# Performance work log

Hardware: AMD Instinct MI355X
Metric: run time of the kernel (lower is better)

Reference implementation:

```python
import jax, jax.numpy as jnp
import numpy as np
import math

D_MODEL = 768
N_HEAD = 12
D_FF = 3072
LN_EPS = 1e-5


def gelu_new(x):
    return 0.5 * x * (1.0 + jnp.tanh(jnp.sqrt(2.0 / jnp.pi) * (x + 0.044715 * x ** 3)))


def layer_norm(x, g, b):
    mu = jnp.mean(x, axis=-1, keepdims=True)
    var = jnp.mean(jnp.square(x - mu), axis=-1, keepdims=True)
    return (x - mu) * jax.lax.rsqrt(var + LN_EPS) * g + b


def setup_inputs() -> dict:
    key = jax.random.key(0)
    ks = jax.random.split(key, 8)
    B, S = 4, 2048
    x = jax.random.normal(ks[0], (B, S, D_MODEL), dtype=jnp.float32)
    # causal look-ahead mask: 1 = attend, 0 = masked
    look_ahead_mask = jnp.tril(jnp.ones((S, S), dtype=jnp.float32))[None, None]
    std = 0.02
    Wqkv = jax.random.normal(ks[1], (D_MODEL, 3 * D_MODEL), dtype=jnp.float32) * std
    bqkv = jnp.zeros((3 * D_MODEL,), dtype=jnp.float32)
    Wo = jax.random.normal(ks[2], (D_MODEL, D_MODEL), dtype=jnp.float32) * std
    bo = jnp.zeros((D_MODEL,), dtype=jnp.float32)
    Wfc = jax.random.normal(ks[3], (D_MODEL, D_FF), dtype=jnp.float32) * std
    bfc = jnp.zeros((D_FF,), dtype=jnp.float32)
    Wpr = jax.random.normal(ks[4], (D_FF, D_MODEL), dtype=jnp.float32) * std
    bpr = jnp.zeros((D_MODEL,), dtype=jnp.float32)
    g1 = jnp.ones((D_MODEL,), dtype=jnp.float32)
    b1 = jnp.zeros((D_MODEL,), dtype=jnp.float32)
    g2 = jnp.ones((D_MODEL,), dtype=jnp.float32)
    b2 = jnp.zeros((D_MODEL,), dtype=jnp.float32)
    return dict(x=x, look_ahead_mask=look_ahead_mask, Wqkv=Wqkv, bqkv=bqkv,
                Wo=Wo, bo=bo, Wfc=Wfc, bfc=bfc, Wpr=Wpr, bpr=bpr,
                g1=g1, b1=b1, g2=g2, b2=b2)


def reference(x, look_ahead_mask, Wqkv, bqkv, Wo, bo, Wfc, bfc, Wpr, bpr, g1, b1, g2, b2):
    B, S, D = x.shape
    dk = D // N_HEAD
    # --- attention sublayer (dropout = identity, eval mode) ---
    nx = layer_norm(x, g1, b1)
    qkv = nx @ Wqkv + bqkv                       # [B,S,3D]
    q, k, v = jnp.split(qkv, 3, axis=-1)
    def heads(t):
        return t.reshape(B, S, N_HEAD, dk).transpose(0, 2, 1, 3)  # [B,H,S,dk]
    q, k, v = heads(q), heads(k), heads(v)
    scores = jnp.einsum('bhqd,bhkd->bhqk', q, k) / jnp.sqrt(jnp.float32(dk))
    scores = scores + (1.0 - look_ahead_mask) * -10000.0
    attn_scores = jax.nn.softmax(scores, axis=-1)  # [B,H,S,S]
    out = jnp.einsum('bhqk,bhkd->bhqd', attn_scores, v)
    out = out.transpose(0, 2, 1, 3).reshape(B, S, D)
    a = out @ Wo + bo
    x = x + a
    # --- MLP sublayer ---
    h = layer_norm(x, g2, b2)
    m = gelu_new(h @ Wfc + bfc) @ Wpr + bpr
    x = x + m
    return (x, attn_scores)
```

## Files before the change

### kernel.cpp

```cpp
#include <hip/hip_runtime.h>
#include <stdint.h>

#define D_MODEL 768
#define NHEAD   12
#define DKH     64
#define SEQ     2048
#define BATCH   4
#define DFF     3072
#define NROWS   (BATCH*SEQ)

typedef __bf16 bf16x8 __attribute__((ext_vector_type(8)));
typedef float  f32x4  __attribute__((ext_vector_type(4)));

__device__ __forceinline__ unsigned short f2bf(float f) {
  union { float f; unsigned int u; } v; v.f = f;
  unsigned int r = v.u + 0x7fffu + ((v.u >> 16) & 1u);
  return (unsigned short)(r >> 16);
}

__device__ __forceinline__ void gl_lds16(const void* g, void* l) {
  __builtin_amdgcn_global_load_lds(
      (__attribute__((address_space(1))) void*)(uintptr_t)g,
      (__attribute__((address_space(3))) void*)(uintptr_t)l, 16, 0, 0);
}

__global__ __launch_bounds__(256) void k_prep(
    const float* __restrict__ Wqkv, const float* __restrict__ Wo,
    const float* __restrict__ Wfc, const float* __restrict__ Wpr,
    unsigned short* __restrict__ WqkvT, unsigned short* __restrict__ WoT,
    unsigned short* __restrict__ WfcT, unsigned short* __restrict__ WprT,
    const float* __restrict__ x, const float* __restrict__ g1,
    const float* __restrict__ b1, unsigned short* __restrict__ nx) {
  int id = blockIdx.x;
  if (id < NROWS) {
    int row = id, t = threadIdx.x;
    const float* xr = x + (size_t)row * D_MODEL;
    float v0 = xr[t], v1 = xr[t + 256], v2 = xr[t + 512];
    float s = v0 + v1 + v2;
    float s2 = v0 * v0 + v1 * v1 + v2 * v2;
#pragma unroll
    for (int off = 32; off >= 1; off >>= 1) {
      s  += __shfl_xor(s, off, 64);
      s2 += __shfl_xor(s2, off, 64);
    }
    __shared__ float rs_[4], rs2_[4];
    int w = t >> 6;
    if ((t & 63) == 0) { rs_[w] = s; rs2_[w] = s2; }
    __syncthreads();
    s  = rs_[0] + rs_[1] + rs_[2] + rs_[3];
    s2 = rs2_[0] + rs2_[1] + rs2_[2] + rs2_[3];
    float mu  = s * (1.0f / D_MODEL);
    float var = s2 * (1.0f / D_MODEL) - mu * mu;
    float rstd = rsqrtf(var + 1e-5f);
    unsigned short* yr = nx + (size_t)row * D_MODEL;
    yr[t]       = f2bf((v0 - mu) * rstd * g1[t]       + b1[t]);
    yr[t + 256] = f2bf((v1 - mu) * rstd * g1[t + 256] + b1[t + 256]);
    yr[t + 512] = f2bf((v2 - mu) * rstd * g1[t + 512] + b1[t + 512]);
  } else {
    int wid = id - NROWS;
    const float* W; unsigned short* Wt; int K, N, tid;
    if (wid < 1728)      { W = Wqkv; Wt = WqkvT; K = 768;  N = 2304; tid = wid; }
    else if (wid < 2304) { W = Wo;   Wt = WoT;   K = 768;  N = 768;  tid = wid - 1728; }
    else if (wid < 4608) { W = Wfc;  Wt = WfcT;  K = 768;  N = 3072; tid = wid - 2304; }
    else                 { W = Wpr;  Wt = WprT;  K = 3072; N = 768;  tid = wid - 4608; }
    int ntn = N / 32;
    int n0 = (tid % ntn) * 32, k0 = (tid / ntn) * 32;

    __shared__ float tile[32][33];
    int c = threadIdx.x & 31, r = threadIdx.x >> 5;
#pragma unroll
    for (int i = 0; i < 4; ++i)
      tile[r + i * 8][c] = W[(size_t)(k0 + r + i * 8) * N + n0 + c];
    __syncthreads();
#pragma unroll
    for (int i = 0; i < 4; ++i)
      Wt[(size_t)(n0 + r + i * 8) * K + k0 + c] = f2bf(tile[c][r + i * 8]);
  }
}

__global__ __launch_bounds__(256) void k_ln(const float* __restrict__ x,
                                            const float* __restrict__ g,
                                            const float* __restrict__ bb,
                                            unsigned short* __restrict__ y) {
  int row = blockIdx.x, t = threadIdx.x;
  const float* xr = x + (size_t)row * D_MODEL;
  float v0 = xr[t], v1 = xr[t + 256], v2 = xr[t + 512];
  float s = v0 + v1 + v2;
  float s2 = v0 * v0 + v1 * v1 + v2 * v2;
#pragma unroll
  for (int off = 32; off >= 1; off >>= 1) {
    s  += __shfl_xor(s, off, 64);
    s2 += __shfl_xor(s2, off, 64);
  }
  __shared__ float rs_[4], rs2_[4];
  int w = t >> 6;
  if ((t & 63) == 0) { rs_[w] = s; rs2_[w] = s2; }
  __syncthreads();
  s  = rs_[0] + rs_[1] + rs_[2] + rs_[3];
  s2 = rs2_[0] + rs2_[1] + rs2_[2] + rs2_[3];
  float mu  = s * (1.0f / D_MODEL);
  float var = s2 * (1.0f / D_MODEL) - mu * mu;
  float rstd = rsqrtf(var + 1e-5f);
  unsigned short* yr = y + (size_t)row * D_MODEL;
  yr[t]       = f2bf((v0 - mu) * rstd * g[t]       + bb[t]);
  yr[t + 256] = f2bf((v1 - mu) * rstd * g[t + 256] + bb[t + 256]);
  yr[t + 512] = f2bf((v2 - mu) * rstd * g[t + 512] + bb[t + 512]);
}

#define EPI_QKV 0
#define EPI_WO  1
#define EPI_FC  2
#define EPI_PR  3

template <int EPI>
__global__ __launch_bounds__(256) void k_gemm(
    const unsigned short* __restrict__ A,
    const unsigned short* __restrict__ Bt,
    const float* __restrict__ bias,
    const float* __restrict__ res,
    float* __restrict__ outf,
    unsigned short* __restrict__ outb,
    unsigned short* __restrict__ qo,
    unsigned short* __restrict__ ko,
    unsigned short* __restrict__ vto,
    int K, int N) {
  __shared__ __align__(16) unsigned char smem[36864];
  unsigned short* As = (unsigned short*)smem;
  unsigned short* Bs = (unsigned short*)(smem + 16384);
  int t = threadIdx.x;
  int l = t & 63, w = t >> 6;
  int wm = w >> 1, wn = w & 1;

  int gx = gridDim.x;
  int nwg = gx * gridDim.y;
  int orig = blockIdx.y * gx + blockIdx.x;
  int wg = (orig & 7) * (nwg >> 3) + (orig >> 3);
  int bx = wg % gx, by = wg / gx;
  int m0 = by * 128, n0 = bx * 128;
  int lr = l & 15, lg = l >> 4;

  const f32x4 fz = {0.0f, 0.0f, 0.0f, 0.0f};
  f32x4 acc[4][4];
#pragma unroll
  for (int i = 0; i < 4; ++i)
#pragma unroll
    for (int j = 0; j < 4; ++j) acc[i][j] = fz;

  int arow = t >> 3;
  int aslot = t & 7;
  const unsigned short* Ag = A + (size_t)(m0 + arow) * K + aslot * 8;
  const unsigned short* Bg = Bt + (size_t)(n0 + arow) * K + aslot * 8;
  int ntile = K >> 6;

  for (int kt = 0; kt < ntile; ++kt) {
    const unsigned short* Agk = Ag + kt * 64;
    const unsigned short* Bgk = Bg + kt * 64;
#pragma unroll
    for (int i = 0; i < 4; ++i)
      gl_lds16(Agk + (size_t)i * 32 * K, As + (i * 256 + t) * 8);
#pragma unroll
    for (int i = 0; i < 4; ++i)
      gl_lds16(Bgk + (size_t)i * 32 * K, Bs + (i * 256 + t) * 8);
    __syncthreads();
#pragma unroll
    for (int ks = 0; ks < 2; ++ks) {
      bf16x8 af[4], bf_[4];
#pragma unroll
      for (int i = 0; i < 4; ++i)
        af[i] = *(const bf16x8*)(As + (wm * 64 + i * 16 + lr) * 64 + ks * 32 + lg * 8);
#pragma unroll
      for (int i = 0; i < 4; ++i)
        bf_[i] = *(const bf16x8*)(Bs + (wn * 64 + i * 16 + lr) * 64 + ks * 32 + lg * 8);
#pragma unroll
      for (int i = 0; i < 4; ++i)
#pragma unroll
        for (int j = 0; j < 4; ++j)
          acc[i][j] = __builtin_amdgcn_mfma_f32_16x16x32_bf16(af[i], bf_[j], acc[i][j], 0, 0, 0);
    }
    __syncthreads();
  }

  int mb = m0 + wm * 64;
  int nb = n0 + wn * 64;

  if constexpr (EPI == EPI_WO || EPI == EPI_PR) {
#pragma unroll
    for (int i = 0; i < 4; ++i)
#pragma unroll
      for (int r = 0; r < 4; ++r) {
        int m = mb + i * 16 + 4 * lg + r;
#pragma unroll
        for (int j = 0; j < 4; ++j) {
          int n = nb + j * 16 + lr;
          outf[(size_t)m * D_MODEL + n] = acc[i][j][r] + bias[n] + res[(size_t)m * D_MODEL + n];
        }
      }
  } else if constexpr (EPI == EPI_FC) {
#pragma unroll
    for (int i = 0; i < 4; ++i)
#pragma unroll
      for (int r = 0; r < 4; ++r) {
        int m = mb + i * 16 + 4 * lg + r;
#pragma unroll
        for (int j = 0; j < 4; ++j) {
          int n = nb + j * 16 + lr;
          float u = acc[i][j][r] + bias[n];
          float c = 0.7978845608028654f * (u + 0.044715f * u * u * u);
          float a2 = fabsf(c);
          float e = __expf(-2.0f * a2);
          float th = (1.0f - e) / (1.0f + e);
          th = (c < 0.0f) ? -th : th;
          outb[(size_t)m * DFF + n] = f2bf(0.5f * u * (1.0f + th));
        }
      }
  } else {
    int region = n0 / 768;
    int b = m0 >> 11;
    if (region < 2) {
      unsigned short* dst = (region == 0) ? qo : ko;
#pragma unroll
      for (int i = 0; i < 4; ++i)
#pragma unroll
        for (int r = 0; r < 4; ++r) {
          int m = mb + i * 16 + 4 * lg + r;
          int s = m & (SEQ - 1);
#pragma unroll
          for (int j = 0; j < 4; ++j) {
            int n = nb + j * 16 + lr;
            int nl = n - region * 768;
            int h = nl >> 6, d = nl & 63;
            dst[(((size_t)(b * NHEAD + h) * SEQ + s) << 6) + d] = f2bf(acc[i][j][r] + bias[n]);
          }
        }
    } else {
      int nl = nb - 1536;
      int h = nl >> 6;
      unsigned short* Tw = (unsigned short*)(smem + w * 9216);
#pragma unroll
      for (int j = 0; j < 4; ++j) {
        int dcol = j * 16 + lr;
        int n = nb + j * 16 + lr;
#pragma unroll
        for (int i = 0; i < 4; ++i)
#pragma unroll
          for (int r = 0; r < 4; ++r)
            Tw[dcol * 72 + i * 16 + 4 * lg + r] = f2bf(acc[i][j][r] + bias[n]);
      }
      __syncthreads();
      int srow = l >> 3, sc = (l & 7) * 8;
      int s0 = mb & (SEQ - 1);
#pragma unroll
      for (int i = 0; i < 8; ++i) {
        int d = i * 8 + srow;
        bf16x8 vv = *(const bf16x8*)(Tw + d * 72 + sc);
        *(bf16x8*)(vto + ((size_t)(b * NHEAD + h) * DKH + d) * SEQ + s0 + sc) = vv;
      }
    }
  }
}

template <int EPI>
__global__ __launch_bounds__(256) void k_gemm_pw(
    const unsigned short* __restrict__ A,
    const unsigned short* __restrict__ Bt,
    const float* __restrict__ bias,
    const float* __restrict__ res,
    float* __restrict__ outf,
    unsigned short* __restrict__ outb,
    int K, int N,
    int npw, int gxe, int pwoff,
    const unsigned short* __restrict__ qp,
    const unsigned short* __restrict__ kp,
    const float* __restrict__ lsumbuf,
    float* __restrict__ attn) {
  __shared__ __align__(16) unsigned char smem[36864];
  int t = threadIdx.x;
  int l = t & 63, w = t >> 6;
  int lr = l & 15, lg = l >> 4;
  const f32x4 fz = {0.0f, 0.0f, 0.0f, 0.0f};

  if ((int)blockIdx.x < npw) {
    unsigned short* Ks = (unsigned short*)smem;
    int idx = blockIdx.x + pwoff;
    int qt = 31 - (idx & 31);
    int bh = idx >> 5;
    int qrow0 = qt * 64 + w * 16;

    const unsigned short* qbase = qp + ((size_t)bh * SEQ + qrow0 + lr) * DKH;
    bf16x8 aq0 = *(const bf16x8*)(qbase + lg * 8);
    bf16x8 aq1 = *(const bf16x8*)(qbase + 32 + lg * 8);

    float invl[4];
#pragma unroll
    for (int r = 0; r < 4; ++r)
      invl[r] = 1.0f / lsumbuf[(size_t)bh * SEQ + qrow0 + 4 * lg + r];

    for (int kt = 0; kt <= qt; ++kt) {
#pragma unroll
      for (int i = 0; i < 2; ++i) {
        int lin = i * 256 + t;
        gl_lds16(kp + ((size_t)bh * SEQ + kt * 64 + (lin >> 3)) * DKH + (lin & 7) * 8,
                 Ks + lin * 8);
      }
      __syncthreads();
      f32x4 sacc[4];
#pragma unroll
      for (int f = 0; f < 4; ++f) sacc[f] = fz;
#pragma unroll
      for (int f = 0; f < 4; ++f) {
        bf16x8 bk0 = *(const bf16x8*)(Ks + (f * 16 + lr) * 64 + lg * 8);
        sacc[f] = __builtin_amdgcn_mfma_f32_16x16x32_bf16(aq0, bk0, sacc[f], 0, 0, 0);
        bf16x8 bk1 = *(const bf16x8*)(Ks + (f * 16 + lr) * 64 + 32 + lg * 8);
        sacc[f] = __builtin_amdgcn_mfma_f32_16x16x32_bf16(aq1, bk1, sacc[f], 0, 0, 0);
      }
#pragma unroll
      for (int r = 0; r < 4; ++r) {
        int qg = qrow0 + 4 * lg + r;
#pragma unroll
        for (int f = 0; f < 4; ++f) {
          int ksg = kt * 64 + f * 16 + lr;
          float p = (ksg <= qg) ? __expf(sacc[f][r] * 0.125f) * invl[r] : 0.0f;
          __builtin_nontemporal_store(p, &attn[((size_t)bh * SEQ + qg) * SEQ + ksg]);
        }
      }
      __syncthreads();
    }

    int zstart = (qt + 1) * 64;
    const f32x4 z4 = {0.f, 0.f, 0.f, 0.f};
#pragma unroll
    for (int r = 0; r < 4; ++r) {
      int qg = qrow0 + 4 * lg + r;
      float* rowp = attn + ((size_t)bh * SEQ + qg) * SEQ;
      for (int c = zstart + lr * 4; c < SEQ; c += 64)
        __builtin_nontemporal_store(z4, (f32x4*)(rowp + c));
    }
    return;
  }

  unsigned short* As = (unsigned short*)smem;
  unsigned short* Bs = (unsigned short*)(smem + 16384);
  int wm = w >> 1, wn = w & 1;
  int orig = blockIdx.x - npw;
  int ngemm = gridDim.x - npw;
  int wg = (orig & 7) * (ngemm >> 3) + (orig >> 3);
  int bx = wg % gxe, by = wg / gxe;
  int m0 = by * 128, n0 = bx * 128;

  f32x4 acc[4][4];
#pragma unroll
  for (int i = 0; i < 4; ++i)
#pragma unroll
    for (int j = 0; j < 4; ++j) acc[i][j] = fz;

  int arow = t >> 3;
  int aslot = t & 7;
  const unsigned short* Ag = A + (size_t)(m0 + arow) * K + aslot * 8;
  const unsigned short* Bg = Bt + (size_t)(n0 + arow) * K + aslot * 8;
  int ntile = K >> 6;

  for (int kt = 0; kt < ntile; ++kt) {
    const unsigned short* Agk = Ag + kt * 64;
    const unsigned short* Bgk = Bg + kt * 64;
#pragma unroll
    for (int i = 0; i < 4; ++i)
      gl_lds16(Agk + (size_t)i * 32 * K, As + (i * 256 + t) * 8);
#pragma unroll
    for (int i = 0; i < 4; ++i)
      gl_lds16(Bgk + (size_t)i * 32 * K, Bs + (i * 256 + t) * 8);
    __syncthreads();
#pragma unroll
    for (int ks = 0; ks < 2; ++ks) {
      bf16x8 af[4], bf_[4];
#pragma unroll
      for (int i = 0; i < 4; ++i)
        af[i] = *(const bf16x8*)(As + (wm * 64 + i * 16 + lr) * 64 + ks * 32 + lg * 8);
#pragma unroll
      for (int i = 0; i < 4; ++i)
        bf_[i] = *(const bf16x8*)(Bs + (wn * 64 + i * 16 + lr) * 64 + ks * 32 + lg * 8);
#pragma unroll
      for (int i = 0; i < 4; ++i)
#pragma unroll
        for (int j = 0; j < 4; ++j)
          acc[i][j] = __builtin_amdgcn_mfma_f32_16x16x32_bf16(af[i], bf_[j], acc[i][j], 0, 0, 0);
    }
    __syncthreads();
  }

  int mb = m0 + wm * 64;
  int nb = n0 + wn * 64;

  if constexpr (EPI == EPI_PR) {
#pragma unroll
    for (int i = 0; i < 4; ++i)
#pragma unroll
      for (int r = 0; r < 4; ++r) {
        int m = mb + i * 16 + 4 * lg + r;
#pragma unroll
        for (int j = 0; j < 4; ++j) {
          int n = nb + j * 16 + lr;
          outf[(size_t)m * D_MODEL + n] = acc[i][j][r] + bias[n] + res[(size_t)m * D_MODEL + n];
        }
      }
  } else {
#pragma unroll
    for (int i = 0; i < 4; ++i)
#pragma unroll
      for (int r = 0; r < 4; ++r) {
        int m = mb + i * 16 + 4 * lg + r;
#pragma unroll
        for (int j = 0; j < 4; ++j) {
          int n = nb + j * 16 + lr;
          float u = acc[i][j][r] + bias[n];
          float c = 0.7978845608028654f * (u + 0.044715f * u * u * u);
          float a2 = fabsf(c);
          float e = __expf(-2.0f * a2);
          float th = (1.0f - e) / (1.0f + e);
          th = (c < 0.0f) ? -th : th;
          outb[(size_t)m * DFF + n] = f2bf(0.5f * u * (1.0f + th));
        }
      }
  }
}

template <int WRITEP>
__global__ __launch_bounds__(256) void k_attn(const unsigned short* __restrict__ q,
                                              const unsigned short* __restrict__ kk,
                                              const unsigned short* __restrict__ vt,
                                              float* __restrict__ lsumbuf,
                                              float* __restrict__ attn,
                                              unsigned short* __restrict__ ao) {
  __shared__ __align__(16) unsigned short Ks[2][64 * 64];
  __shared__ __align__(16) unsigned short Vts[2][64 * 64];
  __shared__ __align__(16) unsigned short Pw[4][32 * 72];
  int t = threadIdx.x, l = t & 63, w = t >> 6;
  int lr = l & 15, lg = l >> 4;
  int qt = gridDim.x - 1 - blockIdx.x;
  int bh = blockIdx.y;
  int q0 = qt * 128;
  int qrow0 = q0 + w * 32;
  int kmax = 2 * qt + 1;

  auto stageK = [&](int kt, int buf) {
#pragma unroll
    for (int i = 0; i < 2; ++i) {
      int lin = i * 256 + t;
      gl_lds16(kk + ((size_t)bh * SEQ + kt * 64 + (lin >> 3)) * DKH + (lin & 7) * 8,
               Ks[buf] + lin * 8);
    }
  };
  auto stageV = [&](int kt, int buf) {
#pragma unroll
    for (int i = 0; i < 2; ++i) {
      int lin = i * 256 + t;
      gl_lds16(vt + ((size_t)bh * DKH + (lin >> 3)) * SEQ + kt * 64 + (lin & 7) * 8,
               Vts[buf] + lin * 8);
    }
  };

  bf16x8 aq[2][2];
#pragma unroll
  for (int m = 0; m < 2; ++m) {
    const unsigned short* qbase = q + ((size_t)bh * SEQ + qrow0 + m * 16 + lr) * DKH;
    aq[m][0] = *(const bf16x8*)(qbase + lg * 8);
    aq[m][1] = *(const bf16x8*)(qbase + 32 + lg * 8);
  }

  const f32x4 fz = {0.0f, 0.0f, 0.0f, 0.0f};
  float lsum[2][4] = {{0.f, 0.f, 0.f, 0.f}, {0.f, 0.f, 0.f, 0.f}};
  f32x4 oacc[2][4];
#pragma unroll
  for (int m = 0; m < 2; ++m)
#pragma unroll
    for (int f = 0; f < 4; ++f) oacc[m][f] = fz;

  unsigned short* Pme = Pw[w];
  stageK(0, 0);
  stageV(0, 0);
  __syncthreads();
  int cur = 0;
  for (int kt = 0; kt <= kmax; ++kt) {
    if (kt < kmax) { stageK(kt + 1, cur ^ 1); stageV(kt + 1, cur ^ 1); }
    const unsigned short* Kc = Ks[cur];
    const unsigned short* Vc = Vts[cur];
#pragma unroll
    for (int m = 0; m < 2; ++m) {
      f32x4 sacc[4];
#pragma unroll
      for (int f = 0; f < 4; ++f) sacc[f] = fz;
#pragma unroll
      for (int f = 0; f < 4; ++f) {
        bf16x8 bk0 = *(const bf16x8*)(Kc + (f * 16 + lr) * 64 + lg * 8);
        sacc[f] = __builtin_amdgcn_mfma_f32_16x16x32_bf16(aq[m][0], bk0, sacc[f], 0, 0, 0);
        bf16x8 bk1 = *(const bf16x8*)(Kc + (f * 16 + lr) * 64 + 32 + lg * 8);
        sacc[f] = __builtin_amdgcn_mfma_f32_16x16x32_bf16(aq[m][1], bk1, sacc[f], 0, 0, 0);
      }
#pragma unroll
      for (int r = 0; r < 4; ++r) {
        int qg = qrow0 + m * 16 + 4 * lg + r;
        float rsum = 0.f;
#pragma unroll
        for (int f = 0; f < 4; ++f) {
          int ksg = kt * 64 + f * 16 + lr;
          float p = (ksg <= qg) ? __expf(sacc[f][r] * 0.125f) : 0.0f;
          rsum += p;
          Pme[(m * 16 + 4 * lg + r) * 72 + f * 16 + lr] = f2bf(p);
        }
        rsum += __shfl_xor(rsum, 1, 64);
        rsum += __shfl_xor(rsum, 2, 64);
        rsum += __shfl_xor(rsum, 4, 64);
        rsum += __shfl_xor(rsum, 8, 64);
        lsum[m][r] += rsum;
      }
    }
#pragma unroll
    for (int ds = 0; ds < 2; ++ds)
#pragma unroll
      for (int m = 0; m < 2; ++m) {
        bf16x8 ap = *(const bf16x8*)(Pme + (m * 16 + lr) * 72 + ds * 32 + lg * 8);
#pragma unroll
        for (int f = 0; f < 4; ++f) {
          bf16x8 bv = *(const bf16x8*)(Vc + (f * 16 + lr) * 64 + ds * 32 + lg * 8);
          oacc[m][f] = __builtin_amdgcn_mfma_f32_16x16x32_bf16(ap, bv, oacc[m][f], 0, 0, 0);
        }
      }
    __syncthreads();
    cur ^= 1;
  }

  float invl[2][4];
#pragma unroll
  for (int m = 0; m < 2; ++m)
#pragma unroll
    for (int r = 0; r < 4; ++r) {
      invl[m][r] = 1.0f / lsum[m][r];
      if (WRITEP == 0 && lr == 0)
        lsumbuf[(size_t)bh * SEQ + qrow0 + m * 16 + 4 * lg + r] = lsum[m][r];
    }

  int b = bh / NHEAD, h = bh % NHEAD;
#pragma unroll
  for (int m = 0; m < 2; ++m)
#pragma unroll
    for (int r = 0; r < 4; ++r) {
      int qg = qrow0 + m * 16 + 4 * lg + r;
#pragma unroll
      for (int f = 0; f < 4; ++f)
        ao[(size_t)(b * SEQ + qg) * D_MODEL + h * DKH + f * 16 + lr] =
            f2bf(oacc[m][f][r] * invl[m][r]);
    }

  if (WRITEP) {
    stageK(0, 0);
    __syncthreads();
    cur = 0;
    for (int kt = 0; kt <= kmax; ++kt) {
      if (kt < kmax) stageK(kt + 1, cur ^ 1);
      const unsigned short* Kc = Ks[cur];
#pragma unroll
      for (int m = 0; m < 2; ++m) {
        f32x4 sacc[4];
#pragma unroll
        for (int f = 0; f < 4; ++f) sacc[f] = fz;
#pragma unroll
        for (int f = 0; f < 4; ++f) {
          bf16x8 bk0 = *(const bf16x8*)(Kc + (f * 16 + lr) * 64 + lg * 8);
          sacc[f] = __builtin_amdgcn_mfma_f32_16x16x32_bf16(aq[m][0], bk0, sacc[f], 0, 0, 0);
          bf16x8 bk1 = *(const bf16x8*)(Kc + (f * 16 + lr) * 64 + 32 + lg * 8);
          sacc[f] = __builtin_amdgcn_mfma_f32_16x16x32_bf16(aq[m][1], bk1, sacc[f], 0, 0, 0);
        }
#pragma unroll
        for (int r = 0; r < 4; ++r) {
          int qg = qrow0 + m * 16 + 4 * lg + r;
#pragma unroll
          for (int f = 0; f < 4; ++f) {
            int ksg = kt * 64 + f * 16 + lr;
            float p = (ksg <= qg) ? __expf(sacc[f][r] * 0.125f) * invl[m][r] : 0.0f;
            __builtin_nontemporal_store(p, &attn[((size_t)bh * SEQ + qg) * SEQ + ksg]);
          }
        }
      }
      __syncthreads();
      cur ^= 1;
    }

    int zstart = q0 + 128;
    const f32x4 z4 = {0.f, 0.f, 0.f, 0.f};
#pragma unroll
    for (int m = 0; m < 2; ++m)
#pragma unroll
      for (int r = 0; r < 4; ++r) {
        int qg = qrow0 + m * 16 + 4 * lg + r;
        float* rowp = attn + ((size_t)bh * SEQ + qg) * SEQ;
        for (int c = zstart + lr * 4; c < SEQ; c += 64)
          __builtin_nontemporal_store(z4, (f32x4*)(rowp + c));
      }
  }
}

__global__ __launch_bounds__(256) void k_pwrite(const unsigned short* __restrict__ q,
                                                const unsigned short* __restrict__ kk,
                                                const float* __restrict__ lsumbuf,
                                                float* __restrict__ attn) {
  __shared__ __align__(16) unsigned short Ks[64 * 64];
  int t = threadIdx.x, l = t & 63, w = t >> 6;
  int lr = l & 15, lg = l >> 4;
  int qt = blockIdx.x, bh = blockIdx.y;
  int qrow0 = qt * 64 + w * 16;

  const unsigned short* qbase = q + ((size_t)bh * SEQ + qrow0 + lr) * DKH;
  bf16x8 aq0 = *(const bf16x8*)(qbase + lg * 8);
  bf16x8 aq1 = *(const bf16x8*)(qbase + 32 + lg * 8);

  float invl[4];
#pragma unroll
  for (int r = 0; r < 4; ++r)
    invl[r] = 1.0f / lsumbuf[(size_t)bh * SEQ + qrow0 + 4 * lg + r];

  const f32x4 fz = {0.0f, 0.0f, 0.0f, 0.0f};
  for (int kt = 0; kt <= qt; ++kt) {
#pragma unroll
    for (int i = 0; i < 2; ++i) {
      int lin = i * 256 + t;
      gl_lds16(kk + ((size_t)bh * SEQ + kt * 64 + (lin >> 3)) * DKH + (lin & 7) * 8,
               Ks + lin * 8);
    }
    __syncthreads();
    f32x4 sacc[4];
#pragma unroll
    for (int f = 0; f < 4; ++f) sacc[f] = fz;
#pragma unroll
    for (int f = 0; f < 4; ++f) {
      bf16x8 bk0 = *(const bf16x8*)(Ks + (f * 16 + lr) * 64 + lg * 8);
      sacc[f] = __builtin_amdgcn_mfma_f32_16x16x32_bf16(aq0, bk0, sacc[f], 0, 0, 0);
      bf16x8 bk1 = *(const bf16x8*)(Ks + (f * 16 + lr) * 64 + 32 + lg * 8);
      sacc[f] = __builtin_amdgcn_mfma_f32_16x16x32_bf16(aq1, bk1, sacc[f], 0, 0, 0);
    }
#pragma unroll
    for (int r = 0; r < 4; ++r) {
      int qg = qrow0 + 4 * lg + r;
#pragma unroll
      for (int f = 0; f < 4; ++f) {
        int ksg = kt * 64 + f * 16 + lr;
        float p = (ksg <= qg) ? __expf(sacc[f][r] * 0.125f) * invl[r] : 0.0f;
        attn[((size_t)bh * SEQ + qg) * SEQ + ksg] = p;
      }
    }
    __syncthreads();
  }

  int zstart = (qt + 1) * 64;
#pragma unroll
  for (int r = 0; r < 4; ++r) {
    int qg = qrow0 + 4 * lg + r;
    float* rowp = attn + ((size_t)bh * SEQ + qg) * SEQ;
    for (int c = zstart + lr * 4; c < SEQ; c += 64)
      *(f32x4*)(rowp + c) = fz;
  }
}

extern "C" void kernel_launch(void* const* d_in, const int* in_sizes, int n_in,
                              void* d_out, int out_size, void* d_ws, size_t ws_size,
                              hipStream_t stream) {
  (void)in_sizes; (void)n_in; (void)out_size;
  const float* x    = (const float*)d_in[0];
  const float* Wqkv = (const float*)d_in[2];
  const float* bqkv = (const float*)d_in[3];
  const float* Wo   = (const float*)d_in[4];
  const float* bo   = (const float*)d_in[5];
  const float* Wfc  = (const float*)d_in[6];
  const float* bfc  = (const float*)d_in[7];
  const float* Wpr  = (const float*)d_in[8];
  const float* bpr  = (const float*)d_in[9];
  const float* g1   = (const float*)d_in[10];
  const float* b1   = (const float*)d_in[11];
  const float* g2   = (const float*)d_in[12];
  const float* b2   = (const float*)d_in[13];

  float* outx = (float*)d_out;
  float* attn = outx + (size_t)NROWS * D_MODEL;

  char* ws = (char*)d_ws;
  dim3 blk(256);

  const size_t NEED_A = 102629376;
  const size_t NEED_B = 77070336;

  if (ws_size >= NEED_A + 65536) {
    unsigned short* qb    = (unsigned short*)(ws + 0);
    unsigned short* kb    = (unsigned short*)(ws + 12582912);
    unsigned short* vtb   = (unsigned short*)(ws + 25165824);
    unsigned short* m1    = (unsigned short*)(ws + 25165824);
    unsigned short* nx    = (unsigned short*)(ws + 75497472);
    unsigned short* ao    = (unsigned short*)(ws + 75497472);
    unsigned short* hb    = (unsigned short*)(ws + 75497472);
    unsigned short* WqkvT = (unsigned short*)(ws + 88080384);
    unsigned short* WoT   = (unsigned short*)(ws + 91619328);
    unsigned short* WfcT  = (unsigned short*)(ws + 92798976);
    unsigned short* WprT  = (unsigned short*)(ws + 97517568);
    float*          lsum  = (float*)(ws + 102236160);
    float*          x1    = outx;

    k_prep<<<dim3(NROWS + 6912), blk, 0, stream>>>(
        Wqkv, Wo, Wfc, Wpr, WqkvT, WoT, WfcT, WprT, x, g1, b1, nx);
    k_gemm<EPI_QKV><<<dim3(18, 64), blk, 0, stream>>>(
        nx, WqkvT, bqkv, nullptr, nullptr, nullptr, qb, kb, vtb, 768, 2304);
    k_attn<0><<<dim3(SEQ / 128, BATCH * NHEAD), blk, 0, stream>>>(
        qb, kb, vtb, lsum, nullptr, ao);
    k_gemm<EPI_WO><<<dim3(6, 64), blk, 0, stream>>>(
        ao, WoT, bo, x, x1, nullptr, nullptr, nullptr, nullptr, 768, 768);
    k_ln<<<NROWS, blk, 0, stream>>>(x1, g2, b2, hb);
    k_gemm_pw<EPI_FC><<<dim3(768 + 1536), blk, 0, stream>>>(
        hb, WfcT, bfc, nullptr, nullptr, m1, 768, 3072,
        768, 24, 0, qb, kb, lsum, attn);
    k_gemm_pw<EPI_PR><<<dim3(768 + 384), blk, 0, stream>>>(
        m1, WprT, bpr, x1, outx, nullptr, 3072, 768,
        768, 6, 768, qb, kb, lsum, attn);
  } else if (ws_size >= NEED_B + 65536) {
    unsigned short* qb    = (unsigned short*)(ws + 0);
    unsigned short* kb    = (unsigned short*)(ws + 12582912);
    unsigned short* vtb   = (unsigned short*)(ws + 25165824);
    unsigned short* m1    = (unsigned short*)(ws + 0);
    unsigned short* nx    = (unsigned short*)(ws + 50331648);
    unsigned short* ao    = (unsigned short*)(ws + 50331648);
    unsigned short* hb    = (unsigned short*)(ws + 50331648);
    unsigned short* WqkvT = (unsigned short*)(ws + 62914560);
    unsigned short* WoT   = (unsigned short*)(ws + 66453504);
    unsigned short* WfcT  = (unsigned short*)(ws + 67633152);
    unsigned short* WprT  = (unsigned short*)(ws + 72351744);
    float*          x1    = outx;

    k_prep<<<dim3(NROWS + 6912), blk, 0, stream>>>(
        Wqkv, Wo, Wfc, Wpr, WqkvT, WoT, WfcT, WprT, x, g1, b1, nx);
    k_gemm<EPI_QKV><<<dim3(18, 64), blk, 0, stream>>>(
        nx, WqkvT, bqkv, nullptr, nullptr, nullptr, qb, kb, vtb, 768, 2304);
    k_attn<1><<<dim3(SEQ / 128, BATCH * NHEAD), blk, 0, stream>>>(
        qb, kb, vtb, nullptr, attn, ao);
    k_gemm<EPI_WO><<<dim3(6, 64), blk, 0, stream>>>(
        ao, WoT, bo, x, x1, nullptr, nullptr, nullptr, nullptr, 768, 768);
    k_ln<<<NROWS, blk, 0, stream>>>(x1, g2, b2, hb);
    k_gemm<EPI_FC><<<dim3(24, 64), blk, 0, stream>>>(
        hb, WfcT, bfc, nullptr, nullptr, m1, nullptr, nullptr, nullptr, 768, 3072);
    k_gemm<EPI_PR><<<dim3(6, 64), blk, 0, stream>>>(
        m1, WprT, bpr, x1, outx, nullptr, nullptr, nullptr, nullptr, 3072, 768);
  } else {
    size_t off = 0;
    auto alloc = [&](size_t bytes) {
      char* p = ws + off;
      off += (bytes + 255) & ~(size_t)255;
      return p;
    };
    unsigned short* qb   = (unsigned short*)alloc((size_t)NROWS * D_MODEL * 2);
    unsigned short* kb   = (unsigned short*)alloc((size_t)NROWS * D_MODEL * 2);
    float*          lsum = (float*)alloc((size_t)BATCH * NHEAD * SEQ * 4);

    char* aws = (char*)attn;
    size_t aoff = 0;
    auto aalloc = [&](size_t bytes) {
      char* p = aws + aoff;
      aoff += (bytes + 255) & ~(size_t)255;
      return p;
    };
    unsigned short* WqkvT = (unsigned short*)aalloc((size_t)2304 * 768 * 2);
    unsigned short* WoT   = (unsigned short*)aalloc((size_t)768 * 768 * 2);
    unsigned short* WfcT  = (unsigned short*)aalloc((size_t)3072 * 768 * 2);
    unsigned short* WprT  = (unsigned short*)aalloc((size_t)768 * 3072 * 2);
    unsigned short* nx    = (unsigned short*)aalloc((size_t)NROWS * D_MODEL * 2);
    unsigned short* vtb   = (unsigned short*)aalloc((size_t)NROWS * D_MODEL * 2);
    unsigned short* ao    = (unsigned short*)aalloc((size_t)NROWS * D_MODEL * 2);
    float*          x1    = (float*)aalloc((size_t)NROWS * D_MODEL * 4);
    unsigned short* hb    = (unsigned short*)aalloc((size_t)NROWS * D_MODEL * 2);
    unsigned short* m1    = (unsigned short*)aalloc((size_t)NROWS * DFF * 2);

    k_prep<<<dim3(NROWS + 6912), blk, 0, stream>>>(
        Wqkv, Wo, Wfc, Wpr, WqkvT, WoT, WfcT, WprT, x, g1, b1, nx);
    k_gemm<EPI_QKV><<<dim3(18, 64), blk, 0, stream>>>(
        nx, WqkvT, bqkv, nullptr, nullptr, nullptr, qb, kb, vtb, 768, 2304);
    k_attn<0><<<dim3(SEQ / 128, BATCH * NHEAD), blk, 0, stream>>>(
        qb, kb, vtb, lsum, nullptr, ao);
    k_gemm<EPI_WO><<<dim3(6, 64), blk, 0, stream>>>(
        ao, WoT, bo, x, x1, nullptr, nullptr, nullptr, nullptr, 768, 768);
    k_ln<<<NROWS, blk, 0, stream>>>(x1, g2, b2, hb);
    k_gemm<EPI_FC><<<dim3(24, 64), blk, 0, stream>>>(
        hb, WfcT, bfc, nullptr, nullptr, m1, nullptr, nullptr, nullptr, 768, 3072);
    k_gemm<EPI_PR><<<dim3(6, 64), blk, 0, stream>>>(
        m1, WprT, bpr, x1, outx, nullptr, nullptr, nullptr, nullptr, 3072, 768);

    k_pwrite<<<dim3(32, BATCH * NHEAD), blk, 0, stream>>>(qb, kb, lsum, attn);
  }
}
```

Before: 574.4 us.

## Enlarge probability-write tiles to 128 rows with double-buffered K staging

The probability-write blocks fused into the FC and projection GEMM launches now each cover 128 query rows instead of 64, with each wave handling two 16-row groups. K tiles are staged into two LDS buffers so the next tile loads while the current one is used. The aim is to halve K reloads, cut block count and hide load latency. The number of write blocks dropped from 768 to 480 and 288, which changes how the work is balanced against the GEMM blocks. The unused standalone k_pwrite fallback path is also removed.

```diff
diff --git a/kernel.cpp b/kernel.cpp
--- a/kernel.cpp
+++ b/kernel.cpp
@@ -280,61 +280,83 @@
   const f32x4 fz = {0.0f, 0.0f, 0.0f, 0.0f};
 
   if ((int)blockIdx.x < npw) {
-    unsigned short* Ks = (unsigned short*)smem;
+    unsigned short* Ks0 = (unsigned short*)smem;
+    unsigned short* Ks1 = (unsigned short*)(smem + 8192);
+    unsigned short* KsB[2] = {Ks0, Ks1};
     int idx = blockIdx.x + pwoff;
-    int qt = 31 - (idx & 31);
-    int bh = idx >> 5;
-    int qrow0 = qt * 64 + w * 16;
-
-    const unsigned short* qbase = qp + ((size_t)bh * SEQ + qrow0 + lr) * DKH;
-    bf16x8 aq0 = *(const bf16x8*)(qbase + lg * 8);
-    bf16x8 aq1 = *(const bf16x8*)(qbase + 32 + lg * 8);
-
-    float invl[4];
-#pragma unroll
-    for (int r = 0; r < 4; ++r)
-      invl[r] = 1.0f / lsumbuf[(size_t)bh * SEQ + qrow0 + 4 * lg + r];
-
-    for (int kt = 0; kt <= qt; ++kt) {
+    int bh = idx >> 4;
+    int qt = 15 - (idx & 15);
+    int q0 = qt * 128;
+    int qrow0 = q0 + w * 32;
+    int kmax = 2 * qt + 1;
+
+    bf16x8 aq[2][2];
+#pragma unroll
+    for (int m = 0; m < 2; ++m) {
+      const unsigned short* qbase = qp + ((size_t)bh * SEQ + qrow0 + m * 16 + lr) * DKH;
+      aq[m][0] = *(const bf16x8*)(qbase + lg * 8);
+      aq[m][1] = *(const bf16x8*)(qbase + 32 + lg * 8);
+    }
+    float invl[2][4];
+#pragma unroll
+    for (int m = 0; m < 2; ++m)
+#pragma unroll
+      for (int r = 0; r < 4; ++r)
+        invl[m][r] = 1.0f / lsumbuf[(size_t)bh * SEQ + qrow0 + m * 16 + 4 * lg + r];
+
+    auto stageK = [&](int kt, int buf) {
 #pragma unroll
       for (int i = 0; i < 2; ++i) {
         int lin = i * 256 + t;
         gl_lds16(kp + ((size_t)bh * SEQ + kt * 64 + (lin >> 3)) * DKH + (lin & 7) * 8,
-                 Ks + lin * 8);
+                 KsB[buf] + lin * 8);
+      }
+    };
+
+    stageK(0, 0);
+    __syncthreads();
+    int cur = 0;
+    for (int kt = 0; kt <= kmax; ++kt) {
+      if (kt < kmax) stageK(kt + 1, cur ^ 1);
+      const unsigned short* Kc = KsB[cur];
+#pragma unroll
+      for (int m = 0; m < 2; ++m) {
+        f32x4 sacc[4];
+#pragma unroll
+        for (int f = 0; f < 4; ++f) sacc[f] = fz;
+#pragma unroll
+        for (int f = 0; f < 4; ++f) {
+          bf16x8 bk0 = *(const bf16x8*)(Kc + (f * 16 + lr) * 64 + lg * 8);
+          sacc[f] = __builtin_amdgcn_mfma_f32_16x16x32_bf16(aq[m][0], bk0, sacc[f], 0, 0, 0);
+          bf16x8 bk1 = *(const bf16x8*)(Kc + (f * 16 + lr) * 64 + 32 + lg * 8);
+          sacc[f] = __builtin_amdgcn_mfma_f32_16x16x32_bf16(aq[m][1], bk1, sacc[f], 0, 0, 0);
+        }
+#pragma unroll
+        for (int r = 0; r < 4; ++r) {
+          int qg = qrow0 + m * 16 + 4 * lg + r;
+#pragma unroll
+          for (int f = 0; f < 4; ++f) {
+            int ksg = kt * 64 + f * 16 + lr;
+            float p = (ksg <= qg) ? __expf(sacc[f][r] * 0.125f) * invl[m][r] : 0.0f;
+            __builtin_nontemporal_store(p, &attn[((size_t)bh * SEQ + qg) * SEQ + ksg]);
+          }
+        }
       }
       __syncthreads();
-      f32x4 sacc[4];
-#pragma unroll
-      for (int f = 0; f < 4; ++f) sacc[f] = fz;
-#pragma unroll
-      for (int f = 0; f < 4; ++f) {
-        bf16x8 bk0 = *(const bf16x8*)(Ks + (f * 16 + lr) * 64 + lg * 8);
-        sacc[f] = __builtin_amdgcn_mfma_f32_16x16x32_bf16(aq0, bk0, sacc[f], 0, 0, 0);
-        bf16x8 bk1 = *(const bf16x8*)(Ks + (f * 16 + lr) * 64 + 32 + lg * 8);
-        sacc[f] = __builtin_amdgcn_mfma_f32_16x16x32_bf16(aq1, bk1, sacc[f], 0, 0, 0);
-      }
+      cur ^= 1;
+    }
+
+    int zstart = q0 + 128;
+    const f32x4 z4 = {0.f, 0.f, 0.f, 0.f};
+#pragma unroll
+    for (int m = 0; m < 2; ++m)
 #pragma unroll
       for (int r = 0; r < 4; ++r) {
-        int qg = qrow0 + 4 * lg + r;
-#pragma unroll
-        for (int f = 0; f < 4; ++f) {
-          int ksg = kt * 64 + f * 16 + lr;
-          float p = (ksg <= qg) ? __expf(sacc[f][r] * 0.125f) * invl[r] : 0.0f;
-          __builtin_nontemporal_store(p, &attn[((size_t)bh * SEQ + qg) * SEQ + ksg]);
-        }
-      }
-      __syncthreads();
-    }
-
-    int zstart = (qt + 1) * 64;
-    const f32x4 z4 = {0.f, 0.f, 0.f, 0.f};
-#pragma unroll
-    for (int r = 0; r < 4; ++r) {
-      int qg = qrow0 + 4 * lg + r;
-      float* rowp = attn + ((size_t)bh * SEQ + qg) * SEQ;
-      for (int c = zstart + lr * 4; c < SEQ; c += 64)
-        __builtin_nontemporal_store(z4, (f32x4*)(rowp + c));
-    }
+        int qg = qrow0 + m * 16 + 4 * lg + r;
+        float* rowp = attn + ((size_t)bh * SEQ + qg) * SEQ;
+        for (int c = zstart + lr * 4; c < SEQ; c += 64)
+          __builtin_nontemporal_store(z4, (f32x4*)(rowp + c));
+      }
     return;
   }
 
@@ -598,67 +620,6 @@
   }
 }
 
-__global__ __launch_bounds__(256) void k_pwrite(const unsigned short* __restrict__ q,
-                                                const unsigned short* __restrict__ kk,
-                                                const float* __restrict__ lsumbuf,
-                                                float* __restrict__ attn) {
-  __shared__ __align__(16) unsigned short Ks[64 * 64];
-  int t = threadIdx.x, l = t & 63, w = t >> 6;
-  int lr = l & 15, lg = l >> 4;
-  int qt = blockIdx.x, bh = blockIdx.y;
-  int qrow0 = qt * 64 + w * 16;
-
-  const unsigned short* qbase = q + ((size_t)bh * SEQ + qrow0 + lr) * DKH;
-  bf16x8 aq0 = *(const bf16x8*)(qbase + lg * 8);
-  bf16x8 aq1 = *(const bf16x8*)(qbase + 32 + lg * 8);
-
-  float invl[4];
-#pragma unroll
-  for (int r = 0; r < 4; ++r)
-    invl[r] = 1.0f / lsumbuf[(size_t)bh * SEQ + qrow0 + 4 * lg + r];
-
-  const f32x4 fz = {0.0f, 0.0f, 0.0f, 0.0f};
-  for (int kt = 0; kt <= qt; ++kt) {
-#pragma unroll
-    for (int i = 0; i < 2; ++i) {
-      int lin = i * 256 + t;
-      gl_lds16(kk + ((size_t)bh * SEQ + kt * 64 + (lin >> 3)) * DKH + (lin & 7) * 8,
-               Ks + lin * 8);
-    }
-    __syncthreads();
-    f32x4 sacc[4];
-#pragma unroll
-    for (int f = 0; f < 4; ++f) sacc[f] = fz;
-#pragma unroll
-    for (int f = 0; f < 4; ++f) {
-      bf16x8 bk0 = *(const bf16x8*)(Ks + (f * 16 + lr) * 64 + lg * 8);
-      sacc[f] = __builtin_amdgcn_mfma_f32_16x16x32_bf16(aq0, bk0, sacc[f], 0, 0, 0);
-      bf16x8 bk1 = *(const bf16x8*)(Ks + (f * 16 + lr) * 64 + 32 + lg * 8);
-      sacc[f] = __builtin_amdgcn_mfma_f32_16x16x32_bf16(aq1, bk1, sacc[f], 0, 0, 0);
-    }
-#pragma unroll
-    for (int r = 0; r < 4; ++r) {
-      int qg = qrow0 + 4 * lg + r;
-#pragma unroll
-      for (int f = 0; f < 4; ++f) {
-        int ksg = kt * 64 + f * 16 + lr;
-        float p = (ksg <= qg) ? __expf(sacc[f][r] * 0.125f) * invl[r] : 0.0f;
-        attn[((size_t)bh * SEQ + qg) * SEQ + ksg] = p;
-      }
-    }
-    __syncthreads();
-  }
-
-  int zstart = (qt + 1) * 64;
-#pragma unroll
-  for (int r = 0; r < 4; ++r) {
-    int qg = qrow0 + 4 * lg + r;
-    float* rowp = attn + ((size_t)bh * SEQ + qg) * SEQ;
-    for (int c = zstart + lr * 4; c < SEQ; c += 64)
-      *(f32x4*)(rowp + c) = fz;
-  }
-}
-
 extern "C" void kernel_launch(void* const* d_in, const int* in_sizes, int n_in,
                               void* d_out, int out_size, void* d_ws, size_t ws_size,
                               hipStream_t stream) {
@@ -710,13 +671,13 @@
     k_gemm<EPI_WO><<<dim3(6, 64), blk, 0, stream>>>(
         ao, WoT, bo, x, x1, nullptr, nullptr, nullptr, nullptr, 768, 768);
     k_ln<<<NROWS, blk, 0, stream>>>(x1, g2, b2, hb);
-    k_gemm_pw<EPI_FC><<<dim3(768 + 1536), blk, 0, stream>>>(
+    k_gemm_pw<EPI_FC><<<dim3(480 + 1536), blk, 0, stream>>>(
         hb, WfcT, bfc, nullptr, nullptr, m1, 768, 3072,
-        768, 24, 0, qb, kb, lsum, attn);
-    k_gemm_pw<EPI_PR><<<dim3(768 + 384), blk, 0, stream>>>(
+        480, 24, 0, qb, kb, lsum, attn);
+    k_gemm_pw<EPI_PR><<<dim3(288 + 384), blk, 0, stream>>>(
         m1, WprT, bpr, x1, outx, nullptr, 3072, 768,
-        768, 6, 768, qb, kb, lsum, attn);
-  } else if (ws_size >= NEED_B + 65536) {
+        288, 6, 480, qb, kb, lsum, attn);
+  } else {
     unsigned short* qb    = (unsigned short*)(ws + 0);
     unsigned short* kb    = (unsigned short*)(ws + 12582912);
     unsigned short* vtb   = (unsigned short*)(ws + 25165824);
@@ -743,49 +704,5 @@
         hb, WfcT, bfc, nullptr, nullptr, m1, nullptr, nullptr, nullptr, 768, 3072);
     k_gemm<EPI_PR><<<dim3(6, 64), blk, 0, stream>>>(
         m1, WprT, bpr, x1, outx, nullptr, nullptr, nullptr, nullptr, 3072, 768);
-  } else {
-    size_t off = 0;
-    auto alloc = [&](size_t bytes) {
-      char* p = ws + off;
-      off += (bytes + 255) & ~(size_t)255;
-      return p;
-    };
-    unsigned short* qb   = (unsigned short*)alloc((size_t)NROWS * D_MODEL * 2);
-    unsigned short* kb   = (unsigned short*)alloc((size_t)NROWS * D_MODEL * 2);
-    float*          lsum = (float*)alloc((size_t)BATCH * NHEAD * SEQ * 4);
-
-    char* aws = (char*)attn;
-    size_t aoff = 0;
-    auto aalloc = [&](size_t bytes) {
-      char* p = aws + aoff;
-      aoff += (bytes + 255) & ~(size_t)255;
-      return p;
-    };
-    unsigned short* WqkvT = (unsigned short*)aalloc((size_t)2304 * 768 * 2);
-    unsigned short* WoT   = (unsigned short*)aalloc((size_t)768 * 768 * 2);
-    unsigned short* WfcT  = (unsigned short*)aalloc((size_t)3072 * 768 * 2);
-    unsigned short* WprT  = (unsigned short*)aalloc((size_t)768 * 3072 * 2);
-    unsigned short* nx    = (unsigned short*)aalloc((size_t)NROWS * D_MODEL * 2);
-    unsigned short* vtb   = (unsigned short*)aalloc((size_t)NROWS * D_MODEL * 2);
-    unsigned short* ao    = (unsigned short*)aalloc((size_t)NROWS * D_MODEL * 2);
-    float*          x1    = (float*)aalloc((size_t)NROWS * D_MODEL * 4);
-    unsigned short* hb    = (unsigned short*)aalloc((size_t)NROWS * D_MODEL * 2);
-    unsigned short* m1    = (unsigned short*)aalloc((size_t)NROWS * DFF * 2);
-
-    k_prep<<<dim3(NROWS + 6912), blk, 0, stream>>>(
-        Wqkv, Wo, Wfc, Wpr, WqkvT, WoT, WfcT, WprT, x, g1, b1, nx);
-    k_gemm<EPI_QKV><<<dim3(18, 64), blk, 0, stream>>>(
-        nx, WqkvT, bqkv, nullptr, nullptr, nullptr, qb, kb, vtb, 768, 2304);
-    k_attn<0><<<dim3(SEQ / 128, BATCH * NHEAD), blk, 0, stream>>>(
-        qb, kb, vtb, lsum, nullptr, ao);
-    k_gemm<EPI_WO><<<dim3(6, 64), blk, 0, stream>>>(
-        ao, WoT, bo, x, x1, nullptr, nullptr, nullptr, nullptr, 768, 768);
-    k_ln<<<NROWS, blk, 0, stream>>>(x1, g2, b2, hb);
-    k_gemm<EPI_FC><<<dim3(24, 64), blk, 0, stream>>>(
-        hb, WfcT, bfc, nullptr, nullptr, m1, nullptr, nullptr, nullptr, 768, 3072);
-    k_gemm<EPI_PR><<<dim3(6, 64), blk, 0, stream>>>(
-        m1, WprT, bpr, x1, outx, nullptr, nullptr, nullptr, nullptr, 3072, 768);
-
-    k_pwrite<<<dim3(32, BATCH * NHEAD), blk, 0, stream>>>(qb, kb, lsum, attn);
   }
 }
```

After: 609.3 us. 6.1% more time.
